# Kernel tuning notes

Measured on AMD Instinct MI355X. Metric: run time of the kernel, lower is better.

Reference implementation:

```python
import jax, jax.numpy as jnp
import numpy as np

STRIDE = 1
DILATION = 2
EPS = 1e-5

def ste_round(x):
    return x + jax.lax.stop_gradient(jnp.round(x) - x)

def quant_act_int8(x):
    # Int8ActPerTensorFloat: per-tensor scale from abs-max statistics
    s = jax.lax.stop_gradient(jnp.maximum(jnp.max(jnp.abs(x)) / 127.0, 1e-8))
    return jnp.clip(ste_round(x / s), -128.0, 127.0) * s

def quant_weight_int8(w):
    # Int8WeightPerTensorFloat: narrow range [-127, 127]
    s = jax.lax.stop_gradient(jnp.maximum(jnp.max(jnp.abs(w)) / 127.0, 1e-8))
    return jnp.clip(ste_round(w / s), -127.0, 127.0) * s

def quant_relu_uint8(x):
    # QuantReLU: Uint8ActPerTensorFloat on relu output
    r = jax.nn.relu(x)
    s = jax.lax.stop_gradient(jnp.maximum(jnp.max(r) / 255.0, 1e-8))
    return jnp.clip(ste_round(r / s), 0.0, 255.0) * s

def conv2d(x, w, stride_h, dil_h):
    return jax.lax.conv_general_dilated(
        x, w, window_strides=(stride_h, 1), padding='VALID',
        rhs_dilation=(dil_h, 1),
        dimension_numbers=('NCHW', 'OIHW', 'NCHW'))

def bn(x, g, b, m, v):
    inv = g / jnp.sqrt(v + EPS)
    return x * inv[None, :, None, None] + (b - m * inv)[None, :, None, None]

def setup_inputs() -> dict:
    key = jax.random.key(0)
    ks = jax.random.split(key, 3)
    B, C, T, W = 16, 128, 2048, 8
    K = 5
    return {
        'x':  jax.random.normal(ks[0], (B, C, T, W), dtype=jnp.float32),
        'w1': jax.random.normal(ks[1], (C, C, K, 1), dtype=jnp.float32) * 0.05,
        'w2': jax.random.normal(ks[2], (C, C, K, 1), dtype=jnp.float32) * 0.05,
        'g1': jnp.ones((C,), jnp.float32), 'b1': jnp.zeros((C,), jnp.float32),
        'm1': jnp.zeros((C,), jnp.float32), 'v1': jnp.ones((C,), jnp.float32),
        'g2': jnp.ones((C,), jnp.float32), 'b2': jnp.zeros((C,), jnp.float32),
        'm2': jnp.zeros((C,), jnp.float32), 'v2': jnp.ones((C,), jnp.float32),
    }

def reference(x, w1, w2, g1, b1, m1, v1, g2, b2, m2, v2):
    wq1 = quant_weight_int8(w1)
    wq2 = quant_weight_int8(w2)
    # pass 1 (dropout is identity in eval)
    h = bn(conv2d(quant_act_int8(x), wq1, STRIDE, DILATION), g1, b1, m1, v1)
    h = bn(conv2d(quant_act_int8(h), wq2, 1, DILATION), g2, b2, m2, v2)
    h = quant_relu_uint8(h)
    # pass 2 (conv1/bn1 then conv2/bn2 reused)
    h = bn(conv2d(quant_act_int8(h), wq1, STRIDE, DILATION), g1, b1, m1, v1)
    h = bn(conv2d(quant_act_int8(h), wq2, 1, DILATION), g2, b2, m2, v2)
    h = quant_relu_uint8(h)
    return h
```

## Files before the change

### kernel.cpp

```cpp
#include <hip/hip_runtime.h>
#include <hip/hip_bf16.h>

typedef unsigned int  u32;
typedef unsigned short u16;
typedef unsigned char u8;
typedef __attribute__((ext_vector_type(8))) short  short8;
typedef __attribute__((ext_vector_type(8))) u16    ushort8;
typedef __attribute__((ext_vector_type(4))) float  f32x4;

#define DEVI __device__ __forceinline__

constexpr int CB = 16;
constexpr int CC = 128;
constexpr int CW = 8;
constexpr int CK = 5;
constexpr int T0g = 2048, T1g = 2040, T2g = 2032, T3g = 2024, T4g = 2016;


DEVI float wred_max(float m){
  #pragma unroll
  for (int off = 32; off; off >>= 1) m = fmaxf(m, __shfl_down(m, off));
  return m;
}
DEVI float slot_max8(const u32* __restrict__ s){
  float m = 0.f;
  #pragma unroll
  for (int i = 0; i < 8; i++) m = fmaxf(m, __uint_as_float(s[i]));
  return m;
}
DEVI u16 f2bf(float q){ return (u16)(__float_as_uint(q) >> 16); }
DEVI float amax4(float4 v){
  return fmaxf(fmaxf(fabsf(v.x), fabsf(v.y)), fmaxf(fabsf(v.z), fabsf(v.w)));
}

__global__ void k_absmax(const float* __restrict__ p, int n4, u32* __restrict__ slots){
  int gid = blockIdx.x * blockDim.x + threadIdx.x;
  int nth = gridDim.x * blockDim.x;
  const float4* p4 = (const float4*)p;
  float m0 = 0.f, m1 = 0.f, m2 = 0.f, m3 = 0.f;
  int i = gid;
  for (; i + 3*nth < n4; i += 4*nth){
    float4 a = p4[i], b = p4[i + nth], c = p4[i + 2*nth], d = p4[i + 3*nth];
    m0 = fmaxf(m0, amax4(a)); m1 = fmaxf(m1, amax4(b));
    m2 = fmaxf(m2, amax4(c)); m3 = fmaxf(m3, amax4(d));
  }
  for (; i < n4; i += nth) m0 = fmaxf(m0, amax4(p4[i]));
  float m = fmaxf(fmaxf(m0, m1), fmaxf(m2, m3));
  m = wred_max(m);
  if ((threadIdx.x & 63) == 0 && m > 0.f) atomicMax(&slots[blockIdx.x & 7], __float_as_uint(m));
}

__global__ void k_wshuf(const float* __restrict__ w, u16* __restrict__ wlay,
                        const u32* __restrict__ wm){
  float s = fmaxf(slot_max8(wm) / 127.0f, 1e-8f);
  int t8 = blockIdx.x * 256 + threadIdx.x;
  int i0 = t8 * 8;
  int lane = (i0 >> 3) & 63, cot = (i0 >> 9) & 7, st = (i0 >> 12) & 3, kk = i0 >> 14;
  int co = cot*16 + (lane & 15), cib = st*32 + (lane >> 4)*8;
  ushort8 pk;
  #pragma unroll
  for (int j = 0; j < 8; j++){
    float q = rintf(w[(co*CC + cib + j)*CK + kk] / s);
    pk[j] = f2bf(fminf(fmaxf(q, -127.f), 127.f));
  }
  ((ushort8*)wlay)[t8] = pk;
}

__global__ __launch_bounds__(256) void k_qtransX(const float* __restrict__ x, u16* __restrict__ qT,
                          const u32* __restrict__ slot, int N){
  __shared__ float tld[64][65];
  int b = blockIdx.z, c0 = blockIdx.y * 64, n0 = blockIdx.x * 64;
  float s = fmaxf(slot_max8(slot) / 127.0f, 1e-8f);
  const float* xb = x + ((size_t)b * CC + c0) * N;
  int tid = threadIdx.x;
  #pragma unroll
  for (int k = 0; k < 4; k++){
    int o = k*256 + tid, r = o >> 4, q = (o & 15) * 4;
    float4 v = *(const float4*)&xb[(size_t)r * N + n0 + q];
    tld[r][q] = v.x; tld[r][q+1] = v.y; tld[r][q+2] = v.z; tld[r][q+3] = v.w;
  }
  __syncthreads();
  u16* qb = qT + (size_t)b * N * CC + c0;
  #pragma unroll
  for (int k = 0; k < 2; k++){
    int o = k*256 + tid, nn = o >> 3, ch = (o & 7) * 8;
    ushort8 pk;
    #pragma unroll
    for (int j = 0; j < 8; j++){
      float q = fminf(fmaxf(rintf(tld[ch+j][nn] / s), -128.f), 127.f);
      pk[j] = f2bf(q);
    }
    *(ushort8*)&qb[(size_t)(n0 + nn) * CC + ch] = pk;
  }
}

__global__ void k_quantE(const float* __restrict__ h, u16* __restrict__ qT,
                         const u32* __restrict__ slot, long n16){
  float s = fmaxf(slot_max8(slot) / 127.0f, 1e-8f);
  long gid = blockIdx.x * (long)blockDim.x + threadIdx.x;
  long nth = (long)gridDim.x * blockDim.x;
  const float4* h4 = (const float4*)h;
  for (long i = gid; i < n16; i += nth){
    float4 v0 = h4[4*i], v1 = h4[4*i+1], v2 = h4[4*i+2], v3 = h4[4*i+3];
    float vs[16] = {v0.x,v0.y,v0.z,v0.w, v1.x,v1.y,v1.z,v1.w,
                    v2.x,v2.y,v2.z,v2.w, v3.x,v3.y,v3.z,v3.w};
    ushort8 pk0, pk1;
    #pragma unroll
    for (int j = 0; j < 8; j++){
      pk0[j] = f2bf(fminf(fmaxf(rintf(vs[j]   / s), -128.f), 127.f));
      pk1[j] = f2bf(fminf(fmaxf(rintf(vs[j+8] / s), -128.f), 127.f));
    }
    ushort8* dst = (ushort8*)qT + 2*i;
    dst[0] = pk0; dst[1] = pk1;
  }
}

__global__ void k_reluQ(const float* __restrict__ h, u16* __restrict__ qT,
                        const u32* __restrict__ slotR, long n16){
  float mr = slot_max8(slotR);
  float sr = fmaxf(mr / 255.0f, 1e-8f);
  float qm = fminf(rintf(mr / sr), 255.f);
  float s3 = fmaxf(qm * sr / 127.0f, 1e-8f);
  long gid = blockIdx.x * (long)blockDim.x + threadIdx.x;
  long nth = (long)gridDim.x * blockDim.x;
  const float4* h4 = (const float4*)h;
  for (long i = gid; i < n16; i += nth){
    float4 v0 = h4[4*i], v1 = h4[4*i+1], v2 = h4[4*i+2], v3 = h4[4*i+3];
    float vs[16] = {v0.x,v0.y,v0.z,v0.w, v1.x,v1.y,v1.z,v1.w,
                    v2.x,v2.y,v2.z,v2.w, v3.x,v3.y,v3.z,v3.w};
    ushort8 pk0, pk1;
    #pragma unroll
    for (int j = 0; j < 16; j++){
      float qr = fminf(fmaxf(rintf(fmaxf(vs[j], 0.f) / sr), 0.f), 255.f);
      float hv = qr * sr;
      float q3 = fminf(fmaxf(rintf(hv / s3), -128.f), 127.f);
      if (j < 8) pk0[j] = f2bf(q3); else pk1[j-8] = f2bf(q3);
    }
    ushort8* dst = (ushort8*)qT + 2*i;
    dst[0] = pk0; dst[1] = pk1;
  }
}

__global__ __launch_bounds__(256, 4)
void k_conv(const u16* __restrict__ qT, const u16* __restrict__ wlay,
            const float* __restrict__ gg, const float* __restrict__ bbt,
            const float* __restrict__ mmu, const float* __restrict__ vvar,
            float* __restrict__ hout,
            const u32* __restrict__ slotA, int smode,
            const u32* __restrict__ wm,
            u32* __restrict__ omax, int relu_mode, int out_nmajor,
            int Tin, int Tout)
{
  __shared__ __align__(16) short lds[192*64];
  __shared__ float s_alpha[CC], s_beta[CC], s_red[4];
  int tid = threadIdx.x;
  int b = blockIdx.y, t0 = blockIdx.x * 16;

  if (tid < CC){
    float inv = gg[tid] / sqrtf(vvar[tid] + 1e-5f);
    float mA = slot_max8(slotA);
    float s_in;
    if (smode == 0){
      s_in = fmaxf(mA / 127.0f, 1e-8f);
    } else {
      float sr = fmaxf(mA / 255.0f, 1e-8f);
      float qm = fminf(rintf(mA / sr), 255.f);
      s_in = fmaxf(qm * sr / 127.0f, 1e-8f);
    }
    float sw = fmaxf(slot_max8(wm) / 127.0f, 1e-8f);
    s_alpha[tid] = s_in * sw * inv;
    s_beta[tid]  = bbt[tid] - mmu[tid] * inv;
  }

  const u16* qb = qT + (size_t)b * Tin * CW * CC;
  int NT = Tin * CW;
  int lane = tid & 63, wv = tid >> 6;
  int wr = wv >> 1, wc = wv & 1;
  int l15 = lane & 15, l4 = lane >> 4;

  f32x4 acc[4][4] = {};
  const short8* wb8 = (const short8*)wlay;

  for (int ph = 0; ph < 2; ph++){
    for (int r = 0; r < 6; r++){
      int ck = r*256 + tid;
      int n  = ck >> 3;
      int p  = ck & 7;
      int src_n = t0*CW + n;
      if (src_n >= NT) src_n = n & 7;
      size_t srcoff = (size_t)src_n * CC + ph*64 + (size_t)((p ^ (n & 7)) * 8);
      __builtin_amdgcn_global_load_lds(
          (const __attribute__((address_space(1))) u32*)(qb + srcoff),
          (__attribute__((address_space(3))) u32*)&lds[ck*8], 16, 0, 0);
    }
    __syncthreads();
    for (int kk = 0; kk < CK; kk++){
      #pragma unroll
      for (int stl = 0; stl < 2; stl++){
        int st = ph*2 + stl;
        short8 afr[4], bfr[4];
        #pragma unroll
        for (int i = 0; i < 4; i++)
          afr[i] = wb8[((kk*4 + st)*8 + wr*4 + i)*64 + lane];
        #pragma unroll
        for (int i = 0; i < 4; i++){
          int nw  = wc*64 + kk*16 + i*16 + l15;
          int off = nw*64 + (((stl*4 + l4) ^ (l15 & 7)) << 3);
          bfr[i] = *(const short8*)&lds[off];
        }
        #pragma unroll
        for (int i = 0; i < 4; i++)
          #pragma unroll
          for (int j = 0; j < 4; j++)
            acc[i][j] = __builtin_amdgcn_mfma_f32_16x16x32_bf16(afr[i], bfr[j], acc[i][j], 0, 0, 0);
      }
    }
    __syncthreads();
  }

  float lmax = 0.f;
  int NO = Tout * CW;
  if (out_nmajor){
    float* hb = hout + (size_t)b * NO * CC;
    #pragma unroll
    for (int i = 0; i < 4; i++){
      int co0 = wr*64 + i*16 + l4*4;
      float a0 = s_alpha[co0],   a1 = s_alpha[co0+1], a2 = s_alpha[co0+2], a3 = s_alpha[co0+3];
      float e0 = s_beta[co0],    e1 = s_beta[co0+1],  e2 = s_beta[co0+2],  e3 = s_beta[co0+3];
      #pragma unroll
      for (int j = 0; j < 4; j++){
        int tn = t0*CW + wc*64 + j*16 + l15;
        if (tn < NO){
          float4 v;
          v.x = acc[i][j][0]*a0 + e0; v.y = acc[i][j][1]*a1 + e1;
          v.z = acc[i][j][2]*a2 + e2; v.w = acc[i][j][3]*a3 + e3;
          *(float4*)&hb[(size_t)tn * CC + co0] = v;
          if (relu_mode)
            lmax = fmaxf(lmax, fmaxf(fmaxf(v.x, v.y), fmaxf(v.z, v.w)));
          else
            lmax = fmaxf(lmax, fmaxf(fmaxf(fabsf(v.x), fabsf(v.y)), fmaxf(fabsf(v.z), fabsf(v.w))));
        }
      }
    }
  } else {
    float* hb = hout + (size_t)b * CC * NO;
    #pragma unroll
    for (int i = 0; i < 4; i++){
      #pragma unroll
      for (int j = 0; j < 4; j++){
        int tn = t0*CW + wc*64 + j*16 + l15;
        #pragma unroll
        for (int r2 = 0; r2 < 4; r2++){
          int co = wr*64 + i*16 + l4*4 + r2;
          if (tn < NO){
            float v = acc[i][j][r2] * s_alpha[co] + s_beta[co];
            hb[(size_t)co * NO + tn] = v;
            lmax = fmaxf(lmax, relu_mode ? fmaxf(v, 0.f) : fabsf(v));
          }
        }
      }
    }
  }
  lmax = wred_max(lmax);
  if (lane == 0) s_red[wv] = lmax;
  __syncthreads();
  if (tid == 0){
    float m = fmaxf(fmaxf(s_red[0], s_red[1]), fmaxf(s_red[2], s_red[3]));
    if (m > 0.f) atomicMax(&omax[blockIdx.x & 7], __float_as_uint(m));
  }
}

__global__ void k_final(const float* __restrict__ h, float* __restrict__ out,
                        const u32* __restrict__ slotR, long n8){
  float s = fmaxf(slot_max8(slotR) / 255.0f, 1e-8f);
  long gid = blockIdx.x * (long)blockDim.x + threadIdx.x;
  long nth = (long)gridDim.x * blockDim.x;
  const float4* h4 = (const float4*)h;
  float4* o4 = (float4*)out;
  for (long i = gid; i < n8; i += nth){
    float4 v0 = h4[2*i], v1 = h4[2*i+1], r0, r1;
    r0.x = fminf(fmaxf(rintf(fmaxf(v0.x, 0.f) / s), 0.f), 255.f) * s;
    r0.y = fminf(fmaxf(rintf(fmaxf(v0.y, 0.f) / s), 0.f), 255.f) * s;
    r0.z = fminf(fmaxf(rintf(fmaxf(v0.z, 0.f) / s), 0.f), 255.f) * s;
    r0.w = fminf(fmaxf(rintf(fmaxf(v0.w, 0.f) / s), 0.f), 255.f) * s;
    r1.x = fminf(fmaxf(rintf(fmaxf(v1.x, 0.f) / s), 0.f), 255.f) * s;
    r1.y = fminf(fmaxf(rintf(fmaxf(v1.y, 0.f) / s), 0.f), 255.f) * s;
    r1.z = fminf(fmaxf(rintf(fmaxf(v1.z, 0.f) / s), 0.f), 255.f) * s;
    r1.w = fminf(fmaxf(rintf(fmaxf(v1.w, 0.f) / s), 0.f), 255.f) * s;
    o4[2*i] = r0; o4[2*i+1] = r1;
  }
}

extern "C" void kernel_launch(void* const* d_in, const int* in_sizes, int n_in,
                              void* d_out, int out_size, void* d_ws, size_t ws_size,
                              hipStream_t stream){
  const float* x  = (const float*)d_in[0];
  const float* w1 = (const float*)d_in[1];
  const float* w2 = (const float*)d_in[2];
  const float* g1 = (const float*)d_in[3];
  const float* b1 = (const float*)d_in[4];
  const float* m1 = (const float*)d_in[5];
  const float* v1 = (const float*)d_in[6];
  const float* g2 = (const float*)d_in[7];
  const float* b2 = (const float*)d_in[8];
  const float* m2 = (const float*)d_in[9];
  const float* v2 = (const float*)d_in[10];

  char* ws   = (char*)d_ws;
  u32*  hdr  = (u32*)ws;
  u16* wl1  = (u16*)(ws + 512);
  u16* wl2  = (u16*)(ws + 512 + 163840);
  u16* qT   = (u16*)(ws + (size_t)(1 << 19));
  float* hbuf = (float*)(ws + (size_t)(1 << 19) + (size_t)67108864);

  hipMemsetAsync(hdr, 0, 256, stream);
  k_absmax<<<20, 256, 0, stream>>>(w1, CC*CC*CK/4, &hdr[40]);
  k_absmax<<<20, 256, 0, stream>>>(w2, CC*CC*CK/4, &hdr[48]);
  k_wshuf<<<40, 256, 0, stream>>>(w1, wl1, &hdr[40]);
  k_wshuf<<<40, 256, 0, stream>>>(w2, wl2, &hdr[48]);
  k_absmax<<<1024, 256, 0, stream>>>(x, CB*CC*T0g*CW/4, &hdr[0]);
  k_qtransX<<<dim3(T0g*CW/64, 2, CB), 256, 0, stream>>>(x, qT, &hdr[0], T0g*CW);
  k_conv<<<dim3(128, CB), 256, 0, stream>>>(qT, wl1, g1, b1, m1, v1, hbuf,
      &hdr[0], 0, &hdr[40], &hdr[8], 0, 1, T0g, T1g);
  k_quantE<<<1024, 256, 0, stream>>>(hbuf, qT, &hdr[8], (long)CB*T1g*CW*CC/16);
  k_conv<<<dim3(127, CB), 256, 0, stream>>>(qT, wl2, g2, b2, m2, v2, hbuf,
      &hdr[8], 0, &hdr[48], &hdr[16], 1, 1, T1g, T2g);
  k_reluQ<<<1024, 256, 0, stream>>>(hbuf, qT, &hdr[16], (long)CB*T2g*CW*CC/16);
  k_conv<<<dim3(127, CB), 256, 0, stream>>>(qT, wl1, g1, b1, m1, v1, hbuf,
      &hdr[16], 1, &hdr[40], &hdr[24], 0, 1, T2g, T3g);
  k_quantE<<<1024, 256, 0, stream>>>(hbuf, qT, &hdr[24], (long)CB*T3g*CW*CC/16);
  k_conv<<<dim3(126, CB), 256, 0, stream>>>(qT, wl2, g2, b2, m2, v2, hbuf,
      &hdr[24], 0, &hdr[48], &hdr[32], 1, 0, T3g, T4g);
  k_final<<<1024, 256, 0, stream>>>(hbuf, (float*)d_out, &hdr[32], (long)CB*CC*T4g*CW/8);
}
```

Baseline: 772.4 us.

## Switch convolution to int8 MFMA with int8 activation and weight buffers

Quantized activations and weights are now stored as int8 instead of bf16-encoded integers, and the conv kernel uses the i32 16x16x64 i8 MFMA instead of the bf16 16x16x32 one. The full 128-channel input tile is loaded into LDS once, so the two-phase loop and its extra barriers go away. This halves intermediate memory traffic and doubles MFMA throughput per instruction, and stays exact because the values are integers in [-128,127]. The occupancy hint of 4 blocks per SM is dropped, and LDS per block stays the same size.

```diff
diff --git a/kernel.cpp b/kernel.cpp
--- a/kernel.cpp
+++ b/kernel.cpp
@@ -4,9 +4,7 @@
 typedef unsigned int  u32;
 typedef unsigned short u16;
 typedef unsigned char u8;
-typedef __attribute__((ext_vector_type(8))) short  short8;
-typedef __attribute__((ext_vector_type(8))) u16    ushort8;
-typedef __attribute__((ext_vector_type(4))) float  f32x4;
+typedef __attribute__((ext_vector_type(4))) int i32x4;
 
 #define DEVI __device__ __forceinline__
 
@@ -28,7 +26,6 @@
   for (int i = 0; i < 8; i++) m = fmaxf(m, __uint_as_float(s[i]));
   return m;
 }
-DEVI u16 f2bf(float q){ return (u16)(__float_as_uint(q) >> 16); }
 DEVI float amax4(float4 v){
   return fmaxf(fmaxf(fabsf(v.x), fabsf(v.y)), fmaxf(fabsf(v.z), fabsf(v.w)));
 }
@@ -50,23 +47,22 @@
   if ((threadIdx.x & 63) == 0 && m > 0.f) atomicMax(&slots[blockIdx.x & 7], __float_as_uint(m));
 }
 
-__global__ void k_wshuf(const float* __restrict__ w, u16* __restrict__ wlay,
+__global__ void k_wshuf(const float* __restrict__ w, char* __restrict__ wlay,
                         const u32* __restrict__ wm){
   float s = fmaxf(slot_max8(wm) / 127.0f, 1e-8f);
-  int t8 = blockIdx.x * 256 + threadIdx.x;
-  int i0 = t8 * 8;
-  int lane = (i0 >> 3) & 63, cot = (i0 >> 9) & 7, st = (i0 >> 12) & 3, kk = i0 >> 14;
-  int co = cot*16 + (lane & 15), cib = st*32 + (lane >> 4)*8;
-  ushort8 pk;
-  #pragma unroll
-  for (int j = 0; j < 8; j++){
+  int t = blockIdx.x * 256 + threadIdx.x;
+  int lane = t & 63, cot = (t >> 6) & 7, ks = (t >> 9) & 1, kk = t >> 10;
+  int co = cot*16 + (lane & 15), cib = ks*64 + (lane >> 4)*16;
+  char __attribute__((aligned(16))) pk[16];
+  #pragma unroll
+  for (int j = 0; j < 16; j++){
     float q = rintf(w[(co*CC + cib + j)*CK + kk] / s);
-    pk[j] = f2bf(fminf(fmaxf(q, -127.f), 127.f));
-  }
-  ((ushort8*)wlay)[t8] = pk;
-}
-
-__global__ __launch_bounds__(256) void k_qtransX(const float* __restrict__ x, u16* __restrict__ qT,
+    pk[j] = (char)fminf(fmaxf(q, -127.f), 127.f);
+  }
+  ((int4*)wlay)[t] = *(const int4*)pk;
+}
+
+__global__ __launch_bounds__(256) void k_qtransX(const float* __restrict__ x, char* __restrict__ qT,
                           const u32* __restrict__ slot, int N){
   __shared__ float tld[64][65];
   int b = blockIdx.z, c0 = blockIdx.y * 64, n0 = blockIdx.x * 64;
@@ -80,21 +76,18 @@
     tld[r][q] = v.x; tld[r][q+1] = v.y; tld[r][q+2] = v.z; tld[r][q+3] = v.w;
   }
   __syncthreads();
-  u16* qb = qT + (size_t)b * N * CC + c0;
-  #pragma unroll
-  for (int k = 0; k < 2; k++){
-    int o = k*256 + tid, nn = o >> 3, ch = (o & 7) * 8;
-    ushort8 pk;
-    #pragma unroll
-    for (int j = 0; j < 8; j++){
-      float q = fminf(fmaxf(rintf(tld[ch+j][nn] / s), -128.f), 127.f);
-      pk[j] = f2bf(q);
-    }
-    *(ushort8*)&qb[(size_t)(n0 + nn) * CC + ch] = pk;
-  }
-}
-
-__global__ void k_quantE(const float* __restrict__ h, u16* __restrict__ qT,
+  char* qb = qT + (size_t)b * N * CC + c0;
+  int nn = tid >> 2, ch = (tid & 3) * 16;
+  char __attribute__((aligned(16))) pk[16];
+  #pragma unroll
+  for (int j = 0; j < 16; j++){
+    float q = fminf(fmaxf(rintf(tld[ch+j][nn] / s), -128.f), 127.f);
+    pk[j] = (char)q;
+  }
+  *(int4*)&qb[(size_t)(n0 + nn) * CC + ch] = *(const int4*)pk;
+}
+
+__global__ void k_quantE(const float* __restrict__ h, char* __restrict__ qT,
                          const u32* __restrict__ slot, long n16){
   float s = fmaxf(slot_max8(slot) / 127.0f, 1e-8f);
   long gid = blockIdx.x * (long)blockDim.x + threadIdx.x;
@@ -104,18 +97,15 @@
     float4 v0 = h4[4*i], v1 = h4[4*i+1], v2 = h4[4*i+2], v3 = h4[4*i+3];
     float vs[16] = {v0.x,v0.y,v0.z,v0.w, v1.x,v1.y,v1.z,v1.w,
                     v2.x,v2.y,v2.z,v2.w, v3.x,v3.y,v3.z,v3.w};
-    ushort8 pk0, pk1;
-    #pragma unroll
-    for (int j = 0; j < 8; j++){
-      pk0[j] = f2bf(fminf(fmaxf(rintf(vs[j]   / s), -128.f), 127.f));
-      pk1[j] = f2bf(fminf(fmaxf(rintf(vs[j+8] / s), -128.f), 127.f));
-    }
-    ushort8* dst = (ushort8*)qT + 2*i;
-    dst[0] = pk0; dst[1] = pk1;
-  }
-}
-
-__global__ void k_reluQ(const float* __restrict__ h, u16* __restrict__ qT,
+    char __attribute__((aligned(16))) pk[16];
+    #pragma unroll
+    for (int j = 0; j < 16; j++)
+      pk[j] = (char)fminf(fmaxf(rintf(vs[j] / s), -128.f), 127.f);
+    ((int4*)qT)[i] = *(const int4*)pk;
+  }
+}
+
+__global__ void k_reluQ(const float* __restrict__ h, char* __restrict__ qT,
                         const u32* __restrict__ slotR, long n16){
   float mr = slot_max8(slotR);
   float sr = fmaxf(mr / 255.0f, 1e-8f);
@@ -128,21 +118,19 @@
     float4 v0 = h4[4*i], v1 = h4[4*i+1], v2 = h4[4*i+2], v3 = h4[4*i+3];
     float vs[16] = {v0.x,v0.y,v0.z,v0.w, v1.x,v1.y,v1.z,v1.w,
                     v2.x,v2.y,v2.z,v2.w, v3.x,v3.y,v3.z,v3.w};
-    ushort8 pk0, pk1;
+    char __attribute__((aligned(16))) pk[16];
     #pragma unroll
     for (int j = 0; j < 16; j++){
       float qr = fminf(fmaxf(rintf(fmaxf(vs[j], 0.f) / sr), 0.f), 255.f);
       float hv = qr * sr;
-      float q3 = fminf(fmaxf(rintf(hv / s3), -128.f), 127.f);
-      if (j < 8) pk0[j] = f2bf(q3); else pk1[j-8] = f2bf(q3);
-    }
-    ushort8* dst = (ushort8*)qT + 2*i;
-    dst[0] = pk0; dst[1] = pk1;
-  }
-}
-
-__global__ __launch_bounds__(256, 4)
-void k_conv(const u16* __restrict__ qT, const u16* __restrict__ wlay,
+      pk[j] = (char)fminf(fmaxf(rintf(hv / s3), -128.f), 127.f);
+    }
+    ((int4*)qT)[i] = *(const int4*)pk;
+  }
+}
+
+__global__ __launch_bounds__(256)
+void k_conv(const char* __restrict__ qT, const char* __restrict__ wlay,
             const float* __restrict__ gg, const float* __restrict__ bbt,
             const float* __restrict__ mmu, const float* __restrict__ vvar,
             float* __restrict__ hout,
@@ -151,10 +139,24 @@
             u32* __restrict__ omax, int relu_mode, int out_nmajor,
             int Tin, int Tout)
 {
-  __shared__ __align__(16) short lds[192*64];
+  __shared__ __align__(16) char lds8[192*128];
   __shared__ float s_alpha[CC], s_beta[CC], s_red[4];
   int tid = threadIdx.x;
   int b = blockIdx.y, t0 = blockIdx.x * 16;
+
+  const char* qb = qT + (size_t)b * Tin * CW * CC;
+  int NT = Tin * CW;
+  for (int r = 0; r < 6; r++){
+    int ck = r*256 + tid;
+    int n  = ck >> 3;
+    int p  = ck & 7;
+    int src_n = t0*CW + n;
+    if (src_n >= NT) src_n = n & 7;
+    size_t so = (size_t)src_n * CC + (size_t)((p ^ (n & 7)) << 4);
+    __builtin_amdgcn_global_load_lds(
+        (const __attribute__((address_space(1))) u32*)(qb + so),
+        (__attribute__((address_space(3))) u32*)&lds8[ck*16], 16, 0, 0);
+  }
 
   if (tid < CC){
     float inv = gg[tid] / sqrtf(vvar[tid] + 1e-5f);
@@ -171,51 +173,33 @@
     s_alpha[tid] = s_in * sw * inv;
     s_beta[tid]  = bbt[tid] - mmu[tid] * inv;
   }
-
-  const u16* qb = qT + (size_t)b * Tin * CW * CC;
-  int NT = Tin * CW;
+  __syncthreads();
+
   int lane = tid & 63, wv = tid >> 6;
   int wr = wv >> 1, wc = wv & 1;
   int l15 = lane & 15, l4 = lane >> 4;
 
-  f32x4 acc[4][4] = {};
-  const short8* wb8 = (const short8*)wlay;
-
-  for (int ph = 0; ph < 2; ph++){
-    for (int r = 0; r < 6; r++){
-      int ck = r*256 + tid;
-      int n  = ck >> 3;
-      int p  = ck & 7;
-      int src_n = t0*CW + n;
-      if (src_n >= NT) src_n = n & 7;
-      size_t srcoff = (size_t)src_n * CC + ph*64 + (size_t)((p ^ (n & 7)) * 8);
-      __builtin_amdgcn_global_load_lds(
-          (const __attribute__((address_space(1))) u32*)(qb + srcoff),
-          (__attribute__((address_space(3))) u32*)&lds[ck*8], 16, 0, 0);
-    }
-    __syncthreads();
-    for (int kk = 0; kk < CK; kk++){
+  i32x4 acc[4][4] = {};
+  const i32x4* wA = (const i32x4*)wlay;
+
+  #pragma unroll
+  for (int s = 0; s < 10; s++){
+    int kk = s >> 1, ks = s & 1;
+    i32x4 af[4], bf[4];
+    #pragma unroll
+    for (int i = 0; i < 4; i++)
+      af[i] = wA[(s*8 + wr*4 + i)*64 + lane];
+    #pragma unroll
+    for (int j = 0; j < 4; j++){
+      int nw  = wc*64 + kk*16 + j*16 + l15;
+      int off = nw*128 + (((ks*4 + l4) ^ (l15 & 7)) << 4);
+      bf[j] = *(const i32x4*)&lds8[off];
+    }
+    #pragma unroll
+    for (int i = 0; i < 4; i++)
       #pragma unroll
-      for (int stl = 0; stl < 2; stl++){
-        int st = ph*2 + stl;
-        short8 afr[4], bfr[4];
-        #pragma unroll
-        for (int i = 0; i < 4; i++)
-          afr[i] = wb8[((kk*4 + st)*8 + wr*4 + i)*64 + lane];
-        #pragma unroll
-        for (int i = 0; i < 4; i++){
-          int nw  = wc*64 + kk*16 + i*16 + l15;
-          int off = nw*64 + (((stl*4 + l4) ^ (l15 & 7)) << 3);
-          bfr[i] = *(const short8*)&lds[off];
-        }
-        #pragma unroll
-        for (int i = 0; i < 4; i++)
-          #pragma unroll
-          for (int j = 0; j < 4; j++)
-            acc[i][j] = __builtin_amdgcn_mfma_f32_16x16x32_bf16(afr[i], bfr[j], acc[i][j], 0, 0, 0);
-      }
-    }
-    __syncthreads();
+      for (int j = 0; j < 4; j++)
+        acc[i][j] = __builtin_amdgcn_mfma_i32_16x16x64_i8(af[i], bf[j], acc[i][j], 0, 0, 0);
   }
 
   float lmax = 0.f;
@@ -232,8 +216,8 @@
         int tn = t0*CW + wc*64 + j*16 + l15;
         if (tn < NO){
           float4 v;
-          v.x = acc[i][j][0]*a0 + e0; v.y = acc[i][j][1]*a1 + e1;
-          v.z = acc[i][j][2]*a2 + e2; v.w = acc[i][j][3]*a3 + e3;
+          v.x = (float)acc[i][j][0]*a0 + e0; v.y = (float)acc[i][j][1]*a1 + e1;
+          v.z = (float)acc[i][j][2]*a2 + e2; v.w = (float)acc[i][j][3]*a3 + e3;
           *(float4*)&hb[(size_t)tn * CC + co0] = v;
           if (relu_mode)
             lmax = fmaxf(lmax, fmaxf(fmaxf(v.x, v.y), fmaxf(v.z, v.w)));
@@ -253,7 +237,7 @@
         for (int r2 = 0; r2 < 4; r2++){
           int co = wr*64 + i*16 + l4*4 + r2;
           if (tn < NO){
-            float v = acc[i][j][r2] * s_alpha[co] + s_beta[co];
+            float v = (float)acc[i][j][r2] * s_alpha[co] + s_beta[co];
             hb[(size_t)co * NO + tn] = v;
             lmax = fmaxf(lmax, relu_mode ? fmaxf(v, 0.f) : fabsf(v));
           }
@@ -308,16 +292,16 @@
 
   char* ws   = (char*)d_ws;
   u32*  hdr  = (u32*)ws;
-  u16* wl1  = (u16*)(ws + 512);
-  u16* wl2  = (u16*)(ws + 512 + 163840);
-  u16* qT   = (u16*)(ws + (size_t)(1 << 19));
-  float* hbuf = (float*)(ws + (size_t)(1 << 19) + (size_t)67108864);
+  char* wl1  = ws + 512;
+  char* wl2  = ws + 512 + 81920;
+  char* qT   = ws + (size_t)(1 << 18);
+  float* hbuf = (float*)(ws + (size_t)(1 << 18) + (size_t)33554432);
 
   hipMemsetAsync(hdr, 0, 256, stream);
   k_absmax<<<20, 256, 0, stream>>>(w1, CC*CC*CK/4, &hdr[40]);
   k_absmax<<<20, 256, 0, stream>>>(w2, CC*CC*CK/4, &hdr[48]);
-  k_wshuf<<<40, 256, 0, stream>>>(w1, wl1, &hdr[40]);
-  k_wshuf<<<40, 256, 0, stream>>>(w2, wl2, &hdr[48]);
+  k_wshuf<<<20, 256, 0, stream>>>(w1, wl1, &hdr[40]);
+  k_wshuf<<<20, 256, 0, stream>>>(w2, wl2, &hdr[48]);
   k_absmax<<<1024, 256, 0, stream>>>(x, CB*CC*T0g*CW/4, &hdr[0]);
   k_qtransX<<<dim3(T0g*CW/64, 2, CB), 256, 0, stream>>>(x, qT, &hdr[0], T0g*CW);
   k_conv<<<dim3(128, CB), 256, 0, stream>>>(qT, wl1, g1, b1, m1, v1, hbuf,
```

Measured after the change: 636.0 us. -17.7%, faster.
